# Optimization experiments

Hardware: AMD Instinct MI355X
Metric: run time of the kernel (lower is better)

The kernel has to match this reference:

```python
import jax, jax.numpy as jnp
import numpy as np

N = 50000    # total nodes in a batched graph
E = 200000   # directed edges (before self loops)
G = 256      # molecules per batch
F_IN = 64    # atom features
H = 4        # gat heads
CH = 128     # hidden_channels (per head)
D = H * CH   # 512, concat width
MLP_H = 128  # hidden_channels * mlp_hidden_factor
NEG_SLOPE = 0.2


def _gat(x, src, dst, W, a_src, a_dst, b, concat):
    """PyG GATConv (eval mode, self loops already added to src/dst)."""
    n = x.shape[0]
    heads, ch = a_src.shape
    h = (x @ W).reshape(n, heads, ch)                       # [N,H,C]
    e = jax.nn.leaky_relu((h * a_src).sum(-1)[src]
                          + (h * a_dst).sum(-1)[dst], NEG_SLOPE)  # [E,H]
    emax = jax.ops.segment_max(e, dst, num_segments=n)
    emax = jnp.where(jnp.isfinite(emax), emax, 0.0)
    p = jnp.exp(e - emax[dst])
    denom = jax.ops.segment_sum(p, dst, num_segments=n)
    alpha = p / (denom[dst] + 1e-16)                        # segment softmax over dst
    out = jax.ops.segment_sum(h[src] * alpha[..., None], dst, num_segments=n)
    out = out.reshape(n, heads * ch) if concat else out.mean(axis=1)
    return out + b


def _encoder(x, edge_index, batch, p):
    n = x.shape[0]
    loop = jnp.arange(n, dtype=edge_index.dtype)            # GATConv add_self_loops=True
    src = jnp.concatenate([edge_index[0], loop])
    dst = jnp.concatenate([edge_index[1], loop])
    x = jax.nn.elu(_gat(x, src, dst, p['W1'], p['as1'], p['ad1'], p['b1'], True))
    x = jax.nn.elu(_gat(x, src, dst, p['W2'], p['as2'], p['ad2'], p['b2'], True))
    x = _gat(x, src, dst, p['W3'], p['as3'], p['ad3'], p['b3'], False)
    emb = jax.ops.segment_max(x, batch, num_segments=G)     # global_max_pool
    return jnp.where(jnp.isfinite(emb), emb, 0.0)


def setup_inputs() -> dict:
    key = jax.random.key(0)
    ks = jax.random.split(key, 24)
    rn = lambda k, s, sc=0.1: jax.random.normal(k, s, jnp.float32) * sc
    return dict(
        x1=rn(ks[0], (N, F_IN), 1.0),
        edge_index1=jax.random.randint(ks[1], (2, E), 0, N, dtype=jnp.int32),
        batch1=jnp.sort(jax.random.randint(ks[2], (N,), 0, G, dtype=jnp.int32)),
        x2=rn(ks[3], (N, F_IN), 1.0),
        edge_index2=jax.random.randint(ks[4], (2, E), 0, N, dtype=jnp.int32),
        batch2=jnp.sort(jax.random.randint(ks[5], (N,), 0, G, dtype=jnp.int32)),
        W1=rn(ks[6], (F_IN, D)), as1=rn(ks[7], (H, CH)), ad1=rn(ks[8], (H, CH)),
        b1=jnp.zeros((D,), jnp.float32),
        W2=rn(ks[9], (D, D)), as2=rn(ks[10], (H, CH)), ad2=rn(ks[11], (H, CH)),
        b2=jnp.zeros((D,), jnp.float32),
        W3=rn(ks[12], (D, CH)), as3=rn(ks[13], (1, CH)), ad3=rn(ks[14], (1, CH)),
        b3=jnp.zeros((CH,), jnp.float32),
        mw1=rn(ks[15], (2 * CH, MLP_H)), mb1=jnp.zeros((MLP_H,), jnp.float32),
        mw2=rn(ks[16], (MLP_H, 1)), mb2=jnp.zeros((1,), jnp.float32),
    )


def reference(x1, edge_index1, batch1, x2, edge_index2, batch2,
              W1, as1, ad1, b1, W2, as2, ad2, b2, W3, as3, ad3, b3,
              mw1, mb1, mw2, mb2):
    p = dict(W1=W1, as1=as1, ad1=ad1, b1=b1,
             W2=W2, as2=as2, ad2=ad2, b2=b2,
             W3=W3, as3=as3, ad3=ad3, b3=b3)
    e1 = _encoder(x1, edge_index1, batch1, p)               # [G, CH]
    e2 = _encoder(x2, edge_index2, batch2, p)               # [G, CH]
    z = jnp.concatenate([e1, e2], axis=-1)                  # [G, 2*CH]
    return jax.nn.relu(z @ mw1 + mb1) @ mw2 + mb2           # [G, 1]
```

## Files before the change

### kernel.cpp

```cpp
#include <hip/hip_runtime.h>
#include <cstdint>

namespace {
constexpr int kN = 50000;
constexpr int kE = 200000;
constexpr int kE2 = kE + kN;
constexpr int kG = 256;
constexpr float kNegSlope = 0.2f;
}

using half8   = __attribute__((ext_vector_type(8))) _Float16;
using floatx4 = __attribute__((ext_vector_type(4))) float;

__device__ __forceinline__ void gld_lds16(const void* g, void* l) {
  __builtin_amdgcn_global_load_lds(
      (const __attribute__((address_space(1))) unsigned int*)g,
      (__attribute__((address_space(3))) unsigned int*)l, 16, 0, 0);
}

__device__ __forceinline__ float fexp(float x) {
  return __builtin_amdgcn_exp2f(x * 1.44269504088896f);
}

template <int OUTF16, int NT>
__global__ __launch_bounds__(256, 4) void gemm_f16(
    const _Float16* __restrict__ A, const _Float16* __restrict__ B,
    void* __restrict__ Cv, int M, int N, int K) {
  __shared__ alignas(16) char smem[16384];
  char* sA = smem;
  char* sB = smem + 8192;
  const int t = threadIdx.x;
  const int w = t >> 6;
  const int l = t & 63;
  int bm, bn;
  if constexpr (NT == 1) {
    bm = blockIdx.x * 128;
    bn = 0;
  } else {
    const int x = blockIdx.x & 7;
    const int s = blockIdx.x >> 3;
    bm = (((s >> 2) << 3) + x) * 128;
    bn = (s & 3) * 128;
    if (bm >= M) return;
  }
  const int wm = (w & 1) * 64;
  const int wn = (w >> 1) * 64;
  const int quad = l >> 4;
  const int lrow = l & 15;

  floatx4 acc[4][4];
#pragma unroll
  for (int mi = 0; mi < 4; ++mi)
#pragma unroll
    for (int ni = 0; ni < 4; ++ni) acc[mi][ni] = (floatx4){0.f, 0.f, 0.f, 0.f};

  for (int k0 = 0; k0 < K; k0 += 32) {
#pragma unroll
    for (int j = 0; j < 2; ++j) {
      const int s = w * 128 + j * 64 + l;
      const int row = ((s >> 6) << 4) + (s & 15);
      const int q = (s >> 4) & 3;
      int ga = bm + row;
      ga = (ga < M) ? ga : (M - 1);
      gld_lds16(A + (size_t)ga * K + k0 + q * 8, sA + s * 16);
      gld_lds16(B + (size_t)(bn + row) * K + k0 + q * 8, sB + s * 16);
    }
    __syncthreads();
    half8 fa[4], fb[4];
#pragma unroll
    for (int mi = 0; mi < 4; ++mi)
      fa[mi] = *(const half8*)(sA + ((wm >> 4) + mi) * 1024 + l * 16);
#pragma unroll
    for (int ni = 0; ni < 4; ++ni)
      fb[ni] = *(const half8*)(sB + ((wn >> 4) + ni) * 1024 + l * 16);
#pragma unroll
    for (int mi = 0; mi < 4; ++mi)
#pragma unroll
      for (int ni = 0; ni < 4; ++ni)
        acc[mi][ni] = __builtin_amdgcn_mfma_f32_16x16x32_f16(fa[mi], fb[ni],
                                                             acc[mi][ni], 0, 0, 0);
    __syncthreads();
  }
  const int colbase = bn + wn + lrow;
#pragma unroll
  for (int mi = 0; mi < 4; ++mi) {
    const int rbase = bm + wm + mi * 16 + quad * 4;
#pragma unroll
    for (int r = 0; r < 4; ++r) {
      const int grow = rbase + r;
      if (grow < M) {
        if constexpr (OUTF16) {
          _Float16* C = (_Float16*)Cv;
#pragma unroll
          for (int ni = 0; ni < 4; ++ni)
            C[(size_t)grow * N + colbase + ni * 16] = (_Float16)acc[mi][ni][r];
        } else {
          float* C = (float*)Cv;
#pragma unroll
          for (int ni = 0; ni < 4; ++ni)
            C[(size_t)grow * N + colbase + ni * 16] = acc[mi][ni][r];
        }
      }
    }
  }
}

__global__ void wt_split_all(const float* __restrict__ W1, _Float16* Th1,
                             const float* __restrict__ W2, _Float16* Th2,
                             const float* __restrict__ W3, _Float16* Th3) {
  int idx = blockIdx.x * blockDim.x + threadIdx.x;
  const float* W;
  _Float16* Th;
  int K, N;
  if (idx < 64 * 512) {
    W = W1; Th = Th1; K = 64; N = 512;
  } else if (idx < 64 * 512 + 512 * 512) {
    idx -= 64 * 512;
    W = W2; Th = Th2; K = 512; N = 512;
  } else if (idx < 64 * 512 + 512 * 512 + 512 * 128) {
    idx -= 64 * 512 + 512 * 512;
    W = W3; Th = Th3; K = 512; N = 128;
  } else {
    return;
  }
  const int k = idx / N;
  const int n = idx - k * N;
  Th[n * K + k] = (_Float16)W[idx];
}

__global__ void prep2(const float* __restrict__ x0, const float* __restrict__ x1,
                      _Float16* __restrict__ Xh, int* __restrict__ cnt,
                      int* __restrict__ total) {
  const int idx = blockIdx.x * blockDim.x + threadIdx.x;
  const int half = kN * 64;
  if (idx < half) Xh[idx] = (_Float16)x0[idx];
  else if (idx < 2 * half) Xh[idx] = (_Float16)x1[idx - half];
  if (idx < 2 * kN) cnt[idx] = 1;
  if (idx == 0) *total = 0;
}
__global__ void prep(const float* __restrict__ X, _Float16* __restrict__ Xh,
                     int* __restrict__ cnt, int* __restrict__ total, int nsplit,
                     int n) {
  const int idx = blockIdx.x * blockDim.x + threadIdx.x;
  if (idx < nsplit) Xh[idx] = (_Float16)X[idx];
  if (idx < n) cnt[idx] = 1;
  if (idx == 0) *total = 0;
}

__global__ void node_alpha8(const _Float16* __restrict__ h,
                            const float* __restrict__ a_src,
                            const float* __restrict__ a_dst,
                            float* __restrict__ asrc,
                            float* __restrict__ adst, int n_nodes) {
  const int gtid = blockIdx.x * blockDim.x + threadIdx.x;
  const int node = gtid >> 6;
  const int lane = threadIdx.x & 63;
  if (node >= n_nodes) return;
  const int head = lane >> 4;
  const half8 hv = *(const half8*)(h + (size_t)node * 512 + lane * 8);
  float s1 = 0.f, s2 = 0.f;
#pragma unroll
  for (int j = 0; j < 8; ++j) {
    const float v = (float)hv[j];
    s1 = fmaf(v, a_src[lane * 8 + j], s1);
    s2 = fmaf(v, a_dst[lane * 8 + j], s2);
  }
#pragma unroll
  for (int off = 1; off < 16; off <<= 1) {
    s1 += __shfl_xor(s1, off);
    s2 += __shfl_xor(s2, off);
  }
  if ((lane & 15) == 0) {
    asrc[node * 4 + head] = s1;
    adst[node * 4 + head] = s2;
  }
}

__global__ void node_alpha_l3(const float* __restrict__ h,
                              const float* __restrict__ a_src,
                              const float* __restrict__ a_dst,
                              float* __restrict__ asrc, float* __restrict__ adst,
                              int n_nodes) {
  const int gtid = blockIdx.x * blockDim.x + threadIdx.x;
  const int node = gtid >> 6;
  const int lane = threadIdx.x & 63;
  if (node >= n_nodes) return;
  const float2 v = *(const float2*)(h + (size_t)node * 128 + lane * 2);
  float s1 = fmaf(v.x, a_src[lane * 2], v.y * a_src[lane * 2 + 1]);
  float s2 = fmaf(v.x, a_dst[lane * 2], v.y * a_dst[lane * 2 + 1]);
#pragma unroll
  for (int off = 1; off < 64; off <<= 1) {
    s1 += __shfl_xor(s1, off);
    s2 += __shfl_xor(s2, off);
  }
  if (lane == 0) {
    asrc[node] = s1;
    adst[node] = s2;
  }
}

__global__ void count_edges2(const int* __restrict__ d0, const int* __restrict__ d1,
                             int* __restrict__ cnt) {
  const int i = blockIdx.x * blockDim.x + threadIdx.x;
  if (i < kE) atomicAdd(&cnt[d0[i]], 1);
  else if (i < 2 * kE) atomicAdd(&cnt[d1[i - kE] + kN], 1);
}
__global__ void fill_edges2(const int* __restrict__ s0, const int* __restrict__ d0,
                            const int* __restrict__ s1, const int* __restrict__ d1,
                            int* __restrict__ cursor, int* __restrict__ csr) {
  const int i = blockIdx.x * blockDim.x + threadIdx.x;
  if (i < kE) {
    const int p = atomicAdd(&cursor[d0[i]], 1);
    csr[p] = s0[i];
  } else if (i < 2 * kE) {
    const int j = i - kE;
    const int p = atomicAdd(&cursor[d1[j] + kN], 1);
    csr[p] = s1[j] + kN;
  }
}
__global__ void count_edges(const int* __restrict__ dst, int* __restrict__ cnt,
                            int ne) {
  const int i = blockIdx.x * blockDim.x + threadIdx.x;
  if (i < ne) atomicAdd(&cnt[dst[i]], 1);
}
__global__ void fill_edges(const int* __restrict__ src, const int* __restrict__ dst,
                           int* __restrict__ cursor, int* __restrict__ csr, int ne) {
  const int i = blockIdx.x * blockDim.x + threadIdx.x;
  if (i < ne) {
    const int p = atomicAdd(&cursor[dst[i]], 1);
    csr[p] = src[i];
  }
}
__global__ void alloc_ranges(const int* __restrict__ cnt, int* __restrict__ start,
                             int* __restrict__ cursor, int* __restrict__ total,
                             int* __restrict__ csr, int n) {
  const int i = blockIdx.x * blockDim.x + threadIdx.x;
  const int lane = threadIdx.x & 63;
  const int v = (i < n) ? cnt[i] : 0;
  int sc = v;
#pragma unroll
  for (int off = 1; off < 64; off <<= 1) {
    const int t = __shfl_up(sc, off);
    if (lane >= off) sc += t;
  }
  const int wtot = __shfl(sc, 63);
  int base = 0;
  if (lane == 63) base = atomicAdd(total, wtot);
  base = __shfl(base, 63);
  const int st = base + sc - v;
  if (i < n) {
    start[i] = st;
    cursor[i] = st + 1;
    csr[st] = i;
  }
}

__global__ void gat_agg4(const _Float16* __restrict__ h,
                         const float* __restrict__ asrc,
                         const float* __restrict__ adst,
                         const int* __restrict__ start, const int* __restrict__ cnt,
                         const int* __restrict__ csr_src,
                         const float* __restrict__ bias,
                         _Float16* __restrict__ outH, int n_nodes) {
  const int gtid = blockIdx.x * blockDim.x + threadIdx.x;
  const int node = gtid >> 6;
  const int lane = threadIdx.x & 63;
  if (node >= n_nodes) return;
  const int ch = lane * 8;
  const int head = lane >> 4;
  const int s = start[node];
  const int c = cnt[node];
  const float ad = adst[node * 4 + head];
  float a0[8], a1[8];
#pragma unroll
  for (int j = 0; j < 8; ++j) { a0[j] = 0.f; a1[j] = 0.f; }
  float d0 = 0.f, d1 = 0.f;
  int i = 0;
  for (; i + 2 <= c; i += 2) {
    const int s0 = csr_src[s + i];
    const int s1 = csr_src[s + i + 1];
    float e0 = asrc[s0 * 4 + head] + ad;
    float e1 = asrc[s1 * 4 + head] + ad;
    e0 = (e0 > 0.f) ? e0 : kNegSlope * e0;
    e1 = (e1 > 0.f) ? e1 : kNegSlope * e1;
    const float w0 = fexp(e0);
    const float w1 = fexp(e1);
    const half8 v0 = *(const half8*)(h + (size_t)s0 * 512 + ch);
    const half8 v1 = *(const half8*)(h + (size_t)s1 * 512 + ch);
    d0 += w0;
    d1 += w1;
#pragma unroll
    for (int j = 0; j < 8; ++j) {
      a0[j] = fmaf(w0, (float)v0[j], a0[j]);
      a1[j] = fmaf(w1, (float)v1[j], a1[j]);
    }
  }
  if (i < c) {
    const int s0 = csr_src[s + i];
    float e0 = asrc[s0 * 4 + head] + ad;
    e0 = (e0 > 0.f) ? e0 : kNegSlope * e0;
    const float w0 = fexp(e0);
    const half8 v0 = *(const half8*)(h + (size_t)s0 * 512 + ch);
    d0 += w0;
#pragma unroll
    for (int j = 0; j < 8; ++j) a0[j] = fmaf(w0, (float)v0[j], a0[j]);
  }
  const float inv = 1.f / (d0 + d1 + 1e-16f);
  half8 H;
#pragma unroll
  for (int j = 0; j < 8; ++j) {
    float v = (a0[j] + a1[j]) * inv + bias[ch + j];
    v = (v > 0.f) ? v : (fexp(v) - 1.f);
    H[j] = (_Float16)v;
  }
  *(half8*)(outH + (size_t)node * 512 + ch) = H;
}

__global__ void gat_agg_l3(const float* __restrict__ h,
                           const float* __restrict__ asrc,
                           const float* __restrict__ adst,
                           const int* __restrict__ start, const int* __restrict__ cnt,
                           const int* __restrict__ csr_src,
                           const float* __restrict__ bias,
                           float* __restrict__ out, int n_nodes) {
  const int gtid = blockIdx.x * blockDim.x + threadIdx.x;
  const int node = gtid >> 6;
  const int lane = threadIdx.x & 63;
  if (node >= n_nodes) return;
  const int s = start[node];
  const int c = cnt[node];
  const float ad = adst[node];
  float2 a0 = make_float2(0.f, 0.f);
  float2 a1 = make_float2(0.f, 0.f);
  float d0 = 0.f, d1 = 0.f;
  int i = 0;
  for (; i + 2 <= c; i += 2) {
    const int s0 = csr_src[s + i];
    const int s1 = csr_src[s + i + 1];
    float e0 = asrc[s0] + ad;
    float e1 = asrc[s1] + ad;
    e0 = (e0 > 0.f) ? e0 : kNegSlope * e0;
    e1 = (e1 > 0.f) ? e1 : kNegSlope * e1;
    const float w0 = fexp(e0);
    const float w1 = fexp(e1);
    const float2 v0 = *(const float2*)(h + (size_t)s0 * 128 + lane * 2);
    const float2 v1 = *(const float2*)(h + (size_t)s1 * 128 + lane * 2);
    d0 += w0;
    d1 += w1;
    a0.x = fmaf(w0, v0.x, a0.x); a1.x = fmaf(w1, v1.x, a1.x);
    a0.y = fmaf(w0, v0.y, a0.y); a1.y = fmaf(w1, v1.y, a1.y);
  }
  if (i < c) {
    const int s0 = csr_src[s + i];
    float e0 = asrc[s0] + ad;
    e0 = (e0 > 0.f) ? e0 : kNegSlope * e0;
    const float w0 = fexp(e0);
    const float2 v0 = *(const float2*)(h + (size_t)s0 * 128 + lane * 2);
    d0 += w0;
    a0.x = fmaf(w0, v0.x, a0.x);
    a0.y = fmaf(w0, v0.y, a0.y);
  }
  const float inv = 1.f / (d0 + d1 + 1e-16f);
  *(float2*)(out + (size_t)node * 128 + lane * 2) =
      make_float2((a0.x + a1.x) * inv + bias[lane * 2],
                  (a0.y + a1.y) * inv + bias[lane * 2 + 1]);
}

__global__ void pool_max(const float* __restrict__ x, const int* __restrict__ batch,
                         float* __restrict__ emb, int n_nodes) {
  __shared__ int lohi[2];
  const int g = blockIdx.x;
  if (threadIdx.x == 0) {
    int lo = 0, hi = n_nodes;
    while (lo < hi) {
      const int mid = (lo + hi) >> 1;
      if (batch[mid] < g) lo = mid + 1; else hi = mid;
    }
    lohi[0] = lo;
    hi = n_nodes;
    while (lo < hi) {
      const int mid = (lo + hi) >> 1;
      if (batch[mid] < g + 1) lo = mid + 1; else hi = mid;
    }
    lohi[1] = lo;
  }
  __syncthreads();
  const int lo = lohi[0], hi = lohi[1];
  const int c = threadIdx.x;
  float m = -1e30f;
  for (int nid = lo; nid < hi; ++nid) m = fmaxf(m, x[(size_t)nid * 128 + c]);
  emb[g * 128 + c] = (lo < hi) ? m : 0.f;
}

__global__ void mlp_head(const float* __restrict__ e1, const float* __restrict__ e2,
                         const float* __restrict__ mw1, const float* __restrict__ mb1,
                         const float* __restrict__ mw2, const float* __restrict__ mb2,
                         float* __restrict__ out) {
  __shared__ float z[256];
  __shared__ float red[128];
  const int g = blockIdx.x;
  const int j = threadIdx.x;
  z[j] = e1[g * 128 + j];
  z[j + 128] = e2[g * 128 + j];
  __syncthreads();
  float acc = mb1[j];
  for (int k = 0; k < 256; ++k) acc = fmaf(z[k], mw1[k * 128 + j], acc);
  acc = fmaxf(acc, 0.f) * mw2[j];
  red[j] = acc;
  __syncthreads();
  for (int s = 64; s > 0; s >>= 1) {
    if (j < s) red[j] += red[j + s];
    __syncthreads();
  }
  if (j == 0) out[g] = red[0] + mb2[0];
}

namespace {
struct Bufs {
  _Float16 *R1h, *R2h;
  float *R1f, *R2f, *asrc, *adst;
  int *cnt, *start, *cursor, *csr, *total;
  _Float16 *Wth1, *Wth2, *Wth3;
  float* emb;
  size_t need;
};

Bufs plan(void* d_ws, int M, int E) {
  Bufs b;
  char* w = (char*)d_ws;
  size_t off = 0;
  auto take = [&](size_t bytes) -> void* {
    void* p = w + off;
    off += (bytes + 255) & ~(size_t)255;
    return p;
  };
  b.R1h = (_Float16*)take((size_t)M * 512 * 2);
  b.R1f = (float*)b.R1h;
  b.R2h = (_Float16*)take((size_t)M * 512 * 2);
  b.R2f = (float*)b.R2h;
  b.asrc = (float*)take((size_t)M * 4 * 4);
  b.adst = (float*)take((size_t)M * 4 * 4);
  b.cnt = (int*)take((size_t)M * 4);
  b.start = (int*)take((size_t)M * 4);
  b.cursor = (int*)take((size_t)M * 4);
  b.csr = (int*)take((size_t)E * 4);
  b.total = (int*)take(256);
  b.Wth1 = (_Float16*)take((size_t)64 * 512 * 2);
  b.Wth2 = (_Float16*)take((size_t)512 * 512 * 2);
  b.Wth3 = (_Float16*)take((size_t)512 * 128 * 2);
  b.emb = (float*)take((size_t)2 * kG * 128 * 4);
  b.need = off;
  return b;
}

void run_layers(const Bufs& b, void* const* d_in, int M, hipStream_t stream) {
  const float* as1 = (const float*)d_in[7];
  const float* ad1 = (const float*)d_in[8];
  const float* b1 = (const float*)d_in[9];
  const float* as2 = (const float*)d_in[11];
  const float* ad2 = (const float*)d_in[12];
  const float* b2 = (const float*)d_in[13];
  const float* as3 = (const float*)d_in[15];
  const float* ad3 = (const float*)d_in[16];
  const float* b3 = (const float*)d_in[17];
  const int nodeBlocks = (M * 64) / 256;
  const int MT = (M + 127) / 128;
  const int MTp = (MT + 7) & ~7;

  gemm_f16<1, 4><<<MTp * 4, 256, 0, stream>>>(b.R1h, b.Wth1, b.R2h, M, 512, 64);
  node_alpha8<<<nodeBlocks, 256, 0, stream>>>(b.R2h, as1, ad1, b.asrc, b.adst, M);
  gat_agg4<<<nodeBlocks, 256, 0, stream>>>(b.R2h, b.asrc, b.adst, b.start, b.cnt,
                                           b.csr, b1, b.R1h, M);
  gemm_f16<1, 4><<<MTp * 4, 256, 0, stream>>>(b.R1h, b.Wth2, b.R2h, M, 512, 512);
  node_alpha8<<<nodeBlocks, 256, 0, stream>>>(b.R2h, as2, ad2, b.asrc, b.adst, M);
  gat_agg4<<<nodeBlocks, 256, 0, stream>>>(b.R2h, b.asrc, b.adst, b.start, b.cnt,
                                           b.csr, b2, b.R1h, M);
  gemm_f16<0, 1><<<MT, 256, 0, stream>>>(b.R1h, b.Wth3, b.R2f, M, 128, 512);
  node_alpha_l3<<<nodeBlocks, 256, 0, stream>>>(b.R2f, as3, ad3, b.asrc, b.adst, M);
  gat_agg_l3<<<nodeBlocks, 256, 0, stream>>>(b.R2f, b.asrc, b.adst, b.start, b.cnt,
                                             b.csr, b3, b.R1f, M);
}
}

extern "C" void kernel_launch(void* const* d_in, const int* in_sizes, int n_in,
                              void* d_out, int out_size, void* d_ws, size_t ws_size,
                              hipStream_t stream) {
  (void)in_sizes; (void)n_in; (void)out_size;
  const float* W1 = (const float*)d_in[6];
  const float* W2 = (const float*)d_in[10];
  const float* W3 = (const float*)d_in[14];
  const float* mw1 = (const float*)d_in[18];
  const float* mb1 = (const float*)d_in[19];
  const float* mw2 = (const float*)d_in[20];
  const float* mb2 = (const float*)d_in[21];

  Bufs bc = plan(d_ws, 2 * kN, 2 * kE2);
  const bool combined = bc.need <= ws_size;
  Bufs b = combined ? bc : plan(d_ws, kN, kE2);

  const int wtot = 64 * 512 + 512 * 512 + 512 * 128;
  wt_split_all<<<(wtot + 255) / 256, 256, 0, stream>>>(W1, b.Wth1, W2, b.Wth2, W3,
                                                       b.Wth3);
  if (combined) {
    const int M = 2 * kN;
    const int* ei0 = (const int*)d_in[1];
    const int* ei1 = (const int*)d_in[4];
    prep2<<<(2 * kN * 64 + 255) / 256, 256, 0, stream>>>(
        (const float*)d_in[0], (const float*)d_in[3], b.R1h, b.cnt, b.total);
    count_edges2<<<(2 * kE + 255) / 256, 256, 0, stream>>>(ei0 + kE, ei1 + kE,
                                                           b.cnt);
    alloc_ranges<<<(M + 255) / 256, 256, 0, stream>>>(b.cnt, b.start, b.cursor,
                                                      b.total, b.csr, M);
    fill_edges2<<<(2 * kE + 255) / 256, 256, 0, stream>>>(ei0, ei0 + kE, ei1,
                                                          ei1 + kE, b.cursor, b.csr);
    run_layers(b, d_in, M, stream);
    for (int enc = 0; enc < 2; ++enc) {
      const int* batch = (const int*)d_in[enc * 3 + 2];
      pool_max<<<kG, 128, 0, stream>>>(b.R1f + (size_t)enc * kN * 128, batch,
                                       b.emb + (size_t)enc * kG * 128, kN);
    }
  } else {
    for (int enc = 0; enc < 2; ++enc) {
      const float* x = (const float*)d_in[enc * 3 + 0];
      const int* ei = (const int*)d_in[enc * 3 + 1];
      const int* batch = (const int*)d_in[enc * 3 + 2];
      prep<<<(kN * 64 + 255) / 256, 256, 0, stream>>>(x, b.R1h, b.cnt, b.total,
                                                      kN * 64, kN);
      count_edges<<<(kE + 255) / 256, 256, 0, stream>>>(ei + kE, b.cnt, kE);
      alloc_ranges<<<(kN + 255) / 256, 256, 0, stream>>>(b.cnt, b.start, b.cursor,
                                                         b.total, b.csr, kN);
      fill_edges<<<(kE + 255) / 256, 256, 0, stream>>>(ei, ei + kE, b.cursor, b.csr,
                                                       kE);
      run_layers(b, d_in, kN, stream);
      pool_max<<<kG, 128, 0, stream>>>(b.R1f, batch, b.emb + (size_t)enc * kG * 128,
                                       kN);
    }
  }
  mlp_head<<<kG, 128, 0, stream>>>(b.emb, b.emb + (size_t)kG * 128, mw1, mb1, mw2,
                                   mb2, (float*)d_out);
}
```

Baseline: 730.3 us.

## Fuse attention logit computation into aggregation and double-buffer GEMM LDS loads

Removes the separate node_alpha kernels. Each aggregation kernel now recomputes the source attention logit from the gathered feature row it already loads, using a wave shuffle reduction per edge, and computes the self-loop term from the destination node's own row. This drops three kernel launches and the asrc/adst round-trips, but adds a shuffle reduction per edge inside the gather loop. Separately, the f16 GEMM gets a two-stage LDS double buffer with explicit vmcnt waits and barriers, so global-to-LDS loads overlap the MFMA work, at the cost of doubling shared memory to 32KB.

```diff
diff --git a/kernel.cpp b/kernel.cpp
--- a/kernel.cpp
+++ b/kernel.cpp
@@ -26,9 +26,7 @@
 __global__ __launch_bounds__(256, 4) void gemm_f16(
     const _Float16* __restrict__ A, const _Float16* __restrict__ B,
     void* __restrict__ Cv, int M, int N, int K) {
-  __shared__ alignas(16) char smem[16384];
-  char* sA = smem;
-  char* sB = smem + 8192;
+  __shared__ alignas(16) char smem[32768];
   const int t = threadIdx.x;
   const int w = t >> 6;
   const int l = t & 63;
@@ -54,7 +52,7 @@
 #pragma unroll
     for (int ni = 0; ni < 4; ++ni) acc[mi][ni] = (floatx4){0.f, 0.f, 0.f, 0.f};
 
-  for (int k0 = 0; k0 < K; k0 += 32) {
+  auto stage = [&](char* sbuf, int k0) {
 #pragma unroll
     for (int j = 0; j < 2; ++j) {
       const int s = w * 128 + j * 64 + l;
@@ -62,10 +60,24 @@
       const int q = (s >> 4) & 3;
       int ga = bm + row;
       ga = (ga < M) ? ga : (M - 1);
-      gld_lds16(A + (size_t)ga * K + k0 + q * 8, sA + s * 16);
-      gld_lds16(B + (size_t)(bn + row) * K + k0 + q * 8, sB + s * 16);
-    }
-    __syncthreads();
+      gld_lds16(A + (size_t)ga * K + k0 + q * 8, sbuf + s * 16);
+      gld_lds16(B + (size_t)(bn + row) * K + k0 + q * 8, sbuf + 8192 + s * 16);
+    }
+  };
+
+  stage(smem, 0);
+  int cur = 0;
+  for (int k0 = 0; k0 < K; k0 += 32) {
+    char* sA = smem + cur * 16384;
+    char* sB = sA + 8192;
+    if (k0 + 32 < K) {
+      stage(smem + ((cur ^ 1) * 16384), k0 + 32);
+      asm volatile("s_waitcnt vmcnt(4)" ::: "memory");
+    } else {
+      asm volatile("s_waitcnt vmcnt(0)" ::: "memory");
+    }
+    __builtin_amdgcn_s_barrier();
+    asm volatile("" ::: "memory");
     half8 fa[4], fb[4];
 #pragma unroll
     for (int mi = 0; mi < 4; ++mi)
@@ -79,7 +91,9 @@
       for (int ni = 0; ni < 4; ++ni)
         acc[mi][ni] = __builtin_amdgcn_mfma_f32_16x16x32_f16(fa[mi], fb[ni],
                                                              acc[mi][ni], 0, 0, 0);
-    __syncthreads();
+    asm volatile("" ::: "memory");
+    __builtin_amdgcn_s_barrier();
+    cur ^= 1;
   }
   const int colbase = bn + wn + lrow;
 #pragma unroll
@@ -147,58 +161,6 @@
   if (idx == 0) *total = 0;
 }
 
-__global__ void node_alpha8(const _Float16* __restrict__ h,
-                            const float* __restrict__ a_src,
-                            const float* __restrict__ a_dst,
-                            float* __restrict__ asrc,
-                            float* __restrict__ adst, int n_nodes) {
-  const int gtid = blockIdx.x * blockDim.x + threadIdx.x;
-  const int node = gtid >> 6;
-  const int lane = threadIdx.x & 63;
-  if (node >= n_nodes) return;
-  const int head = lane >> 4;
-  const half8 hv = *(const half8*)(h + (size_t)node * 512 + lane * 8);
-  float s1 = 0.f, s2 = 0.f;
-#pragma unroll
-  for (int j = 0; j < 8; ++j) {
-    const float v = (float)hv[j];
-    s1 = fmaf(v, a_src[lane * 8 + j], s1);
-    s2 = fmaf(v, a_dst[lane * 8 + j], s2);
-  }
-#pragma unroll
-  for (int off = 1; off < 16; off <<= 1) {
-    s1 += __shfl_xor(s1, off);
-    s2 += __shfl_xor(s2, off);
-  }
-  if ((lane & 15) == 0) {
-    asrc[node * 4 + head] = s1;
-    adst[node * 4 + head] = s2;
-  }
-}
-
-__global__ void node_alpha_l3(const float* __restrict__ h,
-                              const float* __restrict__ a_src,
-                              const float* __restrict__ a_dst,
-                              float* __restrict__ asrc, float* __restrict__ adst,
-                              int n_nodes) {
-  const int gtid = blockIdx.x * blockDim.x + threadIdx.x;
-  const int node = gtid >> 6;
-  const int lane = threadIdx.x & 63;
-  if (node >= n_nodes) return;
-  const float2 v = *(const float2*)(h + (size_t)node * 128 + lane * 2);
-  float s1 = fmaf(v.x, a_src[lane * 2], v.y * a_src[lane * 2 + 1]);
-  float s2 = fmaf(v.x, a_dst[lane * 2], v.y * a_dst[lane * 2 + 1]);
-#pragma unroll
-  for (int off = 1; off < 64; off <<= 1) {
-    s1 += __shfl_xor(s1, off);
-    s2 += __shfl_xor(s2, off);
-  }
-  if (lane == 0) {
-    asrc[node] = s1;
-    adst[node] = s2;
-  }
-}
-
 __global__ void count_edges2(const int* __restrict__ d0, const int* __restrict__ d1,
                              int* __restrict__ cnt) {
   const int i = blockIdx.x * blockDim.x + threadIdx.x;
@@ -256,8 +218,8 @@
 }
 
 __global__ void gat_agg4(const _Float16* __restrict__ h,
-                         const float* __restrict__ asrc,
-                         const float* __restrict__ adst,
+                         const float* __restrict__ a_src,
+                         const float* __restrict__ a_dst,
                          const int* __restrict__ start, const int* __restrict__ cnt,
                          const int* __restrict__ csr_src,
                          const float* __restrict__ bias,
@@ -267,43 +229,91 @@
   const int lane = threadIdx.x & 63;
   if (node >= n_nodes) return;
   const int ch = lane * 8;
-  const int head = lane >> 4;
+  float as_r[8], ad_r[8];
+#pragma unroll
+  for (int j = 0; j < 8; ++j) {
+    as_r[j] = a_src[ch + j];
+    ad_r[j] = a_dst[ch + j];
+  }
   const int s = start[node];
   const int c = cnt[node];
-  const float ad = adst[node * 4 + head];
+  const half8 vs = *(const half8*)(h + (size_t)node * 512 + ch);
+  float fs[8];
+  float t_src = 0.f, t_dst = 0.f;
+#pragma unroll
+  for (int j = 0; j < 8; ++j) {
+    fs[j] = (float)vs[j];
+    t_src = fmaf(fs[j], as_r[j], t_src);
+    t_dst = fmaf(fs[j], ad_r[j], t_dst);
+  }
+#pragma unroll
+  for (int off = 1; off < 16; off <<= 1) {
+    t_src += __shfl_xor(t_src, off);
+    t_dst += __shfl_xor(t_dst, off);
+  }
+  const float ad = t_dst;
+  float es = t_src + ad;
+  es = (es > 0.f) ? es : kNegSlope * es;
+  const float ws = fexp(es);
+  float d0 = ws, d1 = 0.f;
   float a0[8], a1[8];
 #pragma unroll
-  for (int j = 0; j < 8; ++j) { a0[j] = 0.f; a1[j] = 0.f; }
-  float d0 = 0.f, d1 = 0.f;
-  int i = 0;
+  for (int j = 0; j < 8; ++j) {
+    a0[j] = ws * fs[j];
+    a1[j] = 0.f;
+  }
+  int i = 1;
   for (; i + 2 <= c; i += 2) {
     const int s0 = csr_src[s + i];
     const int s1 = csr_src[s + i + 1];
-    float e0 = asrc[s0 * 4 + head] + ad;
-    float e1 = asrc[s1 * 4 + head] + ad;
+    const half8 v0 = *(const half8*)(h + (size_t)s0 * 512 + ch);
+    const half8 v1 = *(const half8*)(h + (size_t)s1 * 512 + ch);
+    float f0[8], f1[8];
+    float t0 = 0.f, t1 = 0.f;
+#pragma unroll
+    for (int j = 0; j < 8; ++j) {
+      f0[j] = (float)v0[j];
+      f1[j] = (float)v1[j];
+      t0 = fmaf(f0[j], as_r[j], t0);
+      t1 = fmaf(f1[j], as_r[j], t1);
+    }
+#pragma unroll
+    for (int off = 1; off < 16; off <<= 1) {
+      t0 += __shfl_xor(t0, off);
+      t1 += __shfl_xor(t1, off);
+    }
+    float e0 = t0 + ad;
+    float e1 = t1 + ad;
     e0 = (e0 > 0.f) ? e0 : kNegSlope * e0;
     e1 = (e1 > 0.f) ? e1 : kNegSlope * e1;
     const float w0 = fexp(e0);
     const float w1 = fexp(e1);
-    const half8 v0 = *(const half8*)(h + (size_t)s0 * 512 + ch);
-    const half8 v1 = *(const half8*)(h + (size_t)s1 * 512 + ch);
     d0 += w0;
     d1 += w1;
 #pragma unroll
     for (int j = 0; j < 8; ++j) {
-      a0[j] = fmaf(w0, (float)v0[j], a0[j]);
-      a1[j] = fmaf(w1, (float)v1[j], a1[j]);
+      a0[j] = fmaf(w0, f0[j], a0[j]);
+      a1[j] = fmaf(w1, f1[j], a1[j]);
     }
   }
   if (i < c) {
     const int s0 = csr_src[s + i];
-    float e0 = asrc[s0 * 4 + head] + ad;
+    const half8 v0 = *(const half8*)(h + (size_t)s0 * 512 + ch);
+    float f0[8];
+    float t0 = 0.f;
+#pragma unroll
+    for (int j = 0; j < 8; ++j) {
+      f0[j] = (float)v0[j];
+      t0 = fmaf(f0[j], as_r[j], t0);
+    }
+#pragma unroll
+    for (int off = 1; off < 16; off <<= 1) t0 += __shfl_xor(t0, off);
+    float e0 = t0 + ad;
     e0 = (e0 > 0.f) ? e0 : kNegSlope * e0;
     const float w0 = fexp(e0);
-    const half8 v0 = *(const half8*)(h + (size_t)s0 * 512 + ch);
     d0 += w0;
 #pragma unroll
-    for (int j = 0; j < 8; ++j) a0[j] = fmaf(w0, (float)v0[j], a0[j]);
+    for (int j = 0; j < 8; ++j) a0[j] = fmaf(w0, f0[j], a0[j]);
   }
   const float inv = 1.f / (d0 + d1 + 1e-16f);
   half8 H;
@@ -317,8 +327,8 @@
 }
 
 __global__ void gat_agg_l3(const float* __restrict__ h,
-                           const float* __restrict__ asrc,
-                           const float* __restrict__ adst,
+                           const float* __restrict__ a_src,
+                           const float* __restrict__ a_dst,
                            const int* __restrict__ start, const int* __restrict__ cnt,
                            const int* __restrict__ csr_src,
                            const float* __restrict__ bias,
@@ -327,24 +337,44 @@
   const int node = gtid >> 6;
   const int lane = threadIdx.x & 63;
   if (node >= n_nodes) return;
+  const float2 asv = *(const float2*)(a_src + lane * 2);
+  const float2 adv = *(const float2*)(a_dst + lane * 2);
   const int s = start[node];
   const int c = cnt[node];
-  const float ad = adst[node];
-  float2 a0 = make_float2(0.f, 0.f);
+  const float2 vs = *(const float2*)(h + (size_t)node * 128 + lane * 2);
+  float t_src = fmaf(vs.x, asv.x, vs.y * asv.y);
+  float t_dst = fmaf(vs.x, adv.x, vs.y * adv.y);
+#pragma unroll
+  for (int off = 1; off < 64; off <<= 1) {
+    t_src += __shfl_xor(t_src, off);
+    t_dst += __shfl_xor(t_dst, off);
+  }
+  const float ad = t_dst;
+  float es = t_src + ad;
+  es = (es > 0.f) ? es : kNegSlope * es;
+  const float ws = fexp(es);
+  float2 a0 = make_float2(ws * vs.x, ws * vs.y);
   float2 a1 = make_float2(0.f, 0.f);
-  float d0 = 0.f, d1 = 0.f;
-  int i = 0;
+  float d0 = ws, d1 = 0.f;
+  int i = 1;
   for (; i + 2 <= c; i += 2) {
     const int s0 = csr_src[s + i];
     const int s1 = csr_src[s + i + 1];
-    float e0 = asrc[s0] + ad;
-    float e1 = asrc[s1] + ad;
+    const float2 v0 = *(const float2*)(h + (size_t)s0 * 128 + lane * 2);
+    const float2 v1 = *(const float2*)(h + (size_t)s1 * 128 + lane * 2);
+    float t0 = fmaf(v0.x, asv.x, v0.y * asv.y);
+    float t1 = fmaf(v1.x, asv.x, v1.y * asv.y);
+#pragma unroll
+    for (int off = 1; off < 64; off <<= 1) {
+      t0 += __shfl_xor(t0, off);
+      t1 += __shfl_xor(t1, off);
+    }
+    float e0 = t0 + ad;
+    float e1 = t1 + ad;
     e0 = (e0 > 0.f) ? e0 : kNegSlope * e0;
     e1 = (e1 > 0.f) ? e1 : kNegSlope * e1;
     const float w0 = fexp(e0);
     const float w1 = fexp(e1);
-    const float2 v0 = *(const float2*)(h + (size_t)s0 * 128 + lane * 2);
-    const float2 v1 = *(const float2*)(h + (size_t)s1 * 128 + lane * 2);
     d0 += w0;
     d1 += w1;
     a0.x = fmaf(w0, v0.x, a0.x); a1.x = fmaf(w1, v1.x, a1.x);
@@ -352,10 +382,13 @@
   }
   if (i < c) {
     const int s0 = csr_src[s + i];
-    float e0 = asrc[s0] + ad;
+    const float2 v0 = *(const float2*)(h + (size_t)s0 * 128 + lane * 2);
+    float t0 = fmaf(v0.x, asv.x, v0.y * asv.y);
+#pragma unroll
+    for (int off = 1; off < 64; off <<= 1) t0 += __shfl_xor(t0, off);
+    float e0 = t0 + ad;
     e0 = (e0 > 0.f) ? e0 : kNegSlope * e0;
     const float w0 = fexp(e0);
-    const float2 v0 = *(const float2*)(h + (size_t)s0 * 128 + lane * 2);
     d0 += w0;
     a0.x = fmaf(w0, v0.x, a0.x);
     a0.y = fmaf(w0, v0.y, a0.y);
@@ -468,16 +501,13 @@
   const int MTp = (MT + 7) & ~7;
 
   gemm_f16<1, 4><<<MTp * 4, 256, 0, stream>>>(b.R1h, b.Wth1, b.R2h, M, 512, 64);
-  node_alpha8<<<nodeBlocks, 256, 0, stream>>>(b.R2h, as1, ad1, b.asrc, b.adst, M);
-  gat_agg4<<<nodeBlocks, 256, 0, stream>>>(b.R2h, b.asrc, b.adst, b.start, b.cnt,
+  gat_agg4<<<nodeBlocks, 256, 0, stream>>>(b.R2h, as1, ad1, b.start, b.cnt,
                                            b.csr, b1, b.R1h, M);
   gemm_f16<1, 4><<<MTp * 4, 256, 0, stream>>>(b.R1h, b.Wth2, b.R2h, M, 512, 512);
-  node_alpha8<<<nodeBlocks, 256, 0, stream>>>(b.R2h, as2, ad2, b.asrc, b.adst, M);
-  gat_agg4<<<nodeBlocks, 256, 0, stream>>>(b.R2h, b.asrc, b.adst, b.start, b.cnt,
+  gat_agg4<<<nodeBlocks, 256, 0, stream>>>(b.R2h, as2, ad2, b.start, b.cnt,
                                            b.csr, b2, b.R1h, M);
   gemm_f16<0, 1><<<MT, 256, 0, stream>>>(b.R1h, b.Wth3, b.R2f, M, 128, 512);
-  node_alpha_l3<<<nodeBlocks, 256, 0, stream>>>(b.R2f, as3, ad3, b.asrc, b.adst, M);
-  gat_agg_l3<<<nodeBlocks, 256, 0, stream>>>(b.R2f, b.asrc, b.adst, b.start, b.cnt,
+  gat_agg_l3<<<nodeBlocks, 256, 0, stream>>>(b.R2f, as3, ad3, b.start, b.cnt,
                                              b.csr, b3, b.R1f, M);
 }
 }
```

After: 703.9 us. 1.04x faster.
